# Kernel tuning notes

Measured on AMD Instinct MI355X. Metric: run time of the kernel, lower is better.

The kernel has to match this reference:

```python
import jax, jax.numpy as jnp
import numpy as np

N = 50000          # nodes
E = 800000         # edges (before self loops)
IN_C = 64
HID = 32
HEADS = 4
HC = HID * HEADS   # 128
OUT_C = 3
NEG_SLOPE = 0.2


def _lin(key, fan_out, fan_in, scale=None):
    if scale is None:
        scale = 1.0 / np.sqrt(fan_in)
    return (jax.random.normal(key, (fan_out, fan_in), dtype=jnp.float32) * scale)


def setup_inputs() -> dict:
    key = jax.random.key(0)
    ks = jax.random.split(key, 24)
    inp = {
        "x": jax.random.normal(ks[0], (N, IN_C), dtype=jnp.float32),
        "edge_index": jax.random.randint(ks[1], (2, E), 0, N, dtype=jnp.int64),
        "edge_attr": jax.random.uniform(ks[2], (E,), dtype=jnp.float32),
        "g1_Wl": _lin(ks[3], HC, IN_C), "g1_bl": jnp.zeros((HC,), jnp.float32),
        "g1_Wr": _lin(ks[4], HC, IN_C), "g1_br": jnp.zeros((HC,), jnp.float32),
        "g1_We": _lin(ks[5], HC, 1),
        "g1_att": jax.random.normal(ks[6], (HEADS, HID), dtype=jnp.float32) / np.sqrt(HID),
        "g1_bias": jnp.zeros((HC,), jnp.float32),
        "g2_Wl": _lin(ks[7], HC, HC), "g2_bl": jnp.zeros((HC,), jnp.float32),
        "g2_Wr": _lin(ks[8], HC, HC), "g2_br": jnp.zeros((HC,), jnp.float32),
        "g2_We": _lin(ks[9], HC, 1),
        "g2_att": jax.random.normal(ks[10], (1, HC), dtype=jnp.float32) / np.sqrt(HC),
        "g2_bias": jnp.zeros((HC,), jnp.float32),
        # residual projection (in_channels != hidden*heads)
        "res1_W": _lin(ks[11], HC, IN_C), "res1_b": jnp.zeros((HC,), jnp.float32),
        # MLP head
        "fc1_W": _lin(ks[12], HID, HC), "fc1_b": jnp.zeros((HID,), jnp.float32),
        "fc2_W": _lin(ks[13], 32, HID), "fc2_b": jnp.zeros((32,), jnp.float32),
        "fc3_W": _lin(ks[14], OUT_C, 32), "fc3_b": jnp.zeros((OUT_C,), jnp.float32),
    }
    return inp


def gatv2_conv(x, src, dst, ea, Wl, bl, Wr, br, We, att, bias, heads, out_c):
    # x: [N, F]; src/dst: [E'] (self loops already appended); ea: [E', 1]
    xl = (x @ Wl.T + bl).reshape(N, heads, out_c)   # lin_l -> source features
    xr = (x @ Wr.T + br).reshape(N, heads, out_c)   # lin_r -> target features
    ee = (ea @ We.T).reshape(-1, heads, out_c)      # lin_edge (no bias)
    xj = xl[src]                                    # [E', H, C] gather
    m = jax.nn.leaky_relu(xj + xr[dst] + ee, NEG_SLOPE)
    alpha = jnp.einsum('ehc,hc->eh', m, att)        # per-edge logits
    amax = jax.ops.segment_max(alpha, dst, num_segments=N)
    ex = jnp.exp(alpha - amax[dst])
    denom = jax.ops.segment_sum(ex, dst, num_segments=N)
    alpha = ex / (denom[dst] + 1e-16)               # segment softmax over incoming edges
    out = jax.ops.segment_sum(xj * alpha[..., None], dst, num_segments=N)
    return out.reshape(N, heads * out_c) + bias


def reference(x, edge_index, edge_attr,
              g1_Wl, g1_bl, g1_Wr, g1_br, g1_We, g1_att, g1_bias,
              g2_Wl, g2_bl, g2_Wr, g2_br, g2_We, g2_att, g2_bias,
              res1_W, res1_b, fc1_W, fc1_b, fc2_W, fc2_b, fc3_W, fc3_b):
    ea = edge_attr.reshape(-1, 1)                   # dim()==1 -> view(-1,1)
    # add self loops; edge_attr fill_value='mean' (PyG default)
    loop = jnp.arange(N)
    src = jnp.concatenate([edge_index[0], loop])
    dst = jnp.concatenate([edge_index[1], loop])
    ea_mean = jnp.mean(ea, axis=0, keepdims=True)
    ea_full = jnp.concatenate([ea, jnp.broadcast_to(ea_mean, (N, 1))], axis=0)

    h = gatv2_conv(x, src, dst, ea_full, g1_Wl, g1_bl, g1_Wr, g1_br,
                   g1_We, g1_att, g1_bias, HEADS, HID)
    h = jax.nn.elu(h + (x @ res1_W.T + res1_b))     # residual (projected) + ELU

    h2 = gatv2_conv(h, src, dst, ea_full, g2_Wl, g2_bl, g2_Wr, g2_br,
                    g2_We, g2_att, g2_bias, 1, HC)
    h2 = jax.nn.elu(h2 + h)                         # identity residual + ELU

    y = jax.nn.relu(h2 @ fc1_W.T + fc1_b)
    y = jax.nn.relu(y @ fc2_W.T + fc2_b)
    return y @ fc3_W.T + fc3_b                      # [N, 3]
```

## Files before the change

kernel.cpp:

```cpp
#include <hip/hip_runtime.h>
#include <math.h>


typedef short s16x8 __attribute__((ext_vector_type(8)));
typedef float f32x4 __attribute__((ext_vector_type(4)));
typedef float f32x2 __attribute__((ext_vector_type(2)));

__device__ inline unsigned short f2bf(float x) {
  unsigned int u = __float_as_uint(x);
  return (unsigned short)((u + 0x7fffu + ((u >> 16) & 1u)) >> 16);
}
__device__ inline float bf2f(unsigned short h) {
  return __uint_as_float(((unsigned int)h) << 16);
}
__device__ inline float bflo(unsigned int u) { return __uint_as_float(u << 16); }
__device__ inline float bfhi(unsigned int u) { return __uint_as_float(u & 0xffff0000u); }

template <int CTRL>
__device__ inline float dpp_addf(float x) {
  int y = __builtin_amdgcn_update_dpp(0, __float_as_int(x), CTRL, 0xf, 0xf, false);
  return x + __int_as_float(y);
}

__global__ __launch_bounds__(256) void hist_mean(
    const int* __restrict__ ei, const float* __restrict__ ea,
    int* __restrict__ hist, float* __restrict__ partials,
    int E, int Ep, int CH, int NB) {
  __shared__ int h[256];
  __shared__ float red[256];
  int t = threadIdx.x, c = blockIdx.x;
  h[t] = 0;
  float s = 0.f;
  __syncthreads();
  int s0 = c * CH, e_ = min(Ep, s0 + CH);
  for (int e = s0 + t; e < e_; e += 256) {
    int d;
    if (e < E) { d = ei[E + e]; s += ea[e]; }
    else       { d = e - E; }
    atomicAdd(&h[d >> 8], 1);
  }
  red[t] = s;
  __syncthreads();
  for (int ofs = 128; ofs > 0; ofs >>= 1) {
    if (t < ofs) red[t] += red[t + ofs];
    __syncthreads();
  }
  if (t == 0) partials[c] = red[0];
  for (int k = t; k < NB; k += 256) hist[(size_t)k * gridDim.x + c] = h[k];
}

__global__ __launch_bounds__(256) void mean_final_kernel(
    const float* __restrict__ partials, float* __restrict__ meanv, int E) {
  __shared__ float red[256];
  red[threadIdx.x] = partials[threadIdx.x];
  __syncthreads();
  for (int ofs = 128; ofs > 0; ofs >>= 1) {
    if (threadIdx.x < ofs) red[threadIdx.x] += red[threadIdx.x + ofs];
    __syncthreads();
  }
  if (threadIdx.x == 0) meanv[0] = red[0] / (float)E;
}

__global__ __launch_bounds__(1024) void scan_blocksum(
    const int* __restrict__ in, int* __restrict__ blksum, int n) {
  __shared__ int ws[16];
  int t = threadIdx.x;
  int base = blockIdx.x * 4096 + t * 4;
  int s = 0;
  if (base + 3 < n) {
    int4 v = *(const int4*)(in + base);
    s = v.x + v.y + v.z + v.w;
  } else {
    for (int i = 0; i < 4; i++) if (base + i < n) s += in[base + i];
  }
  int lane = t & 63, w = t >> 6;
#pragma unroll
  for (int ofs = 1; ofs < 64; ofs <<= 1) s += __shfl_xor(s, ofs);
  if (lane == 0) ws[w] = s;
  __syncthreads();
  if (t == 0) {
    int tot = 0;
#pragma unroll
    for (int i = 0; i < 16; i++) tot += ws[i];
    blksum[blockIdx.x] = tot;
  }
}

__global__ __launch_bounds__(64) void scan_blkoff(int* __restrict__ blksum, int nb) {
  int t = threadIdx.x;
  int v = (t < nb) ? blksum[t] : 0;
  int orig = v;
#pragma unroll
  for (int ofs = 1; ofs < 64; ofs <<= 1) {
    int u = __shfl_up(v, ofs);
    if (t >= ofs) v += u;
  }
  if (t < nb) blksum[t] = v - orig;
}

__global__ __launch_bounds__(1024) void scan_out(
    const int* __restrict__ in, const int* __restrict__ blksum,
    int* __restrict__ out, int n, int total) {
  __shared__ int ws[16];
  int t = threadIdx.x;
  int base = blockIdx.x * 4096 + t * 4;
  int4 v = {0, 0, 0, 0};
  if (base + 3 < n) {
    v = *(const int4*)(in + base);
  } else {
    if (base + 0 < n) v.x = in[base + 0];
    if (base + 1 < n) v.y = in[base + 1];
    if (base + 2 < n) v.z = in[base + 2];
    if (base + 3 < n) v.w = in[base + 3];
  }
  int s = v.x + v.y + v.z + v.w;
  int lane = t & 63, w = t >> 6;
  int inc = s;
#pragma unroll
  for (int ofs = 1; ofs < 64; ofs <<= 1) {
    int u = __shfl_up(inc, ofs);
    if (lane >= ofs) inc += u;
  }
  if (lane == 63) ws[w] = inc;
  __syncthreads();
  int waveoff = 0;
#pragma unroll
  for (int i = 0; i < 16; i++) waveoff += (i < w) ? ws[i] : 0;
  int excl = blksum[blockIdx.x] + waveoff + inc - s;
  int p0 = excl, p1 = p0 + v.x, p2 = p1 + v.y, p3 = p2 + v.z;
  if (base + 0 < n) out[base + 0] = p0;
  if (base + 1 < n) out[base + 1] = p1;
  if (base + 2 < n) out[base + 2] = p2;
  if (base + 3 < n) out[base + 3] = p3;
  if (blockIdx.x == 0 && t == 0) out[n] = total;
}

__global__ __launch_bounds__(256) void bin_scatter(
    const int* __restrict__ ei, const float* __restrict__ ea,
    const float* __restrict__ meanv, const int* __restrict__ histoff,
    unsigned int* __restrict__ binmeta, unsigned char* __restrict__ bindlo,
    int E, int Ep, int CH, int NB) {
  __shared__ int off[256];
  int t = threadIdx.x, c = blockIdx.x;
  for (int k = t; k < NB; k += 256) off[k] = histoff[(size_t)k * gridDim.x + c];
  __syncthreads();
  int s = c * CH, e_ = min(Ep, s + CH);
  for (int e = s + t; e < e_; e += 256) {
    int d, src; float eav;
    if (e < E) { src = ei[e]; d = ei[E + e]; eav = ea[e]; }
    else       { src = d = e - E; eav = meanv[0]; }
    int pos = atomicAdd(&off[d >> 8], 1);
    binmeta[pos] = (unsigned int)src | ((unsigned int)f2bf(eav) << 16);
    bindlo[pos] = (unsigned char)(d & 255);
  }
}

__global__ __launch_bounds__(256) void bin_finalize(
    const unsigned int* __restrict__ binmeta, const unsigned char* __restrict__ bindlo,
    const int* __restrict__ histoff, unsigned int* __restrict__ meta,
    int* __restrict__ row_ptr, int N, int Ep, int NCHUNK, int NB) {
  __shared__ int cntl[256];
  __shared__ int ws4[4];
  int t = threadIdx.x, k = blockIdx.x;
  int kstart = histoff[(size_t)k * NCHUNK];
  int kend = (k == NB - 1) ? Ep : histoff[(size_t)(k + 1) * NCHUNK];
  cntl[t] = 0;
  __syncthreads();
  for (int i = kstart + t; i < kend; i += 256) atomicAdd(&cntl[bindlo[i]], 1);
  __syncthreads();
  int v = cntl[t];
  int lane = t & 63, w = t >> 6;
  int inc = v;
#pragma unroll
  for (int ofs = 1; ofs < 64; ofs <<= 1) {
    int u = __shfl_up(inc, ofs);
    if (lane >= ofs) inc += u;
  }
  if (lane == 63) ws4[w] = inc;
  __syncthreads();
  int waveoff = 0;
#pragma unroll
  for (int i = 0; i < 4; i++) waveoff += (i < w) ? ws4[i] : 0;
  int base = kstart + waveoff + inc - v;
  int gd = k * 256 + t;
  if (gd < N) row_ptr[gd] = base;
  if (k == 0 && t == 0) row_ptr[N] = Ep;
  __syncthreads();
  cntl[t] = base;
  __syncthreads();
  for (int i = kstart + t; i < kend; i += 256) {
    int d = bindlo[i];
    int pos = atomicAdd(&cntl[d], 1);
    meta[pos] = binmeta[i];
  }
}

template <int K, int NMAT, int INBF>
__global__ __launch_bounds__(256) void gemm_mfma(
    const void* __restrict__ Xv,
    const float* __restrict__ W0, const float* __restrict__ b0, unsigned short* __restrict__ o0,
    const float* __restrict__ W1, const float* __restrict__ b1, unsigned short* __restrict__ o1,
    const float* __restrict__ W2, const float* __restrict__ b2, unsigned short* __restrict__ o2,
    int N) {
  constexpr int KS = K / 32;
  __shared__ unsigned short Xhi[32 * K];
  __shared__ unsigned short Xlo[INBF ? 1 : 32 * K];
  int t = threadIdx.x;
  int m0 = blockIdx.x * 32;
  int which = (NMAT == 1) ? 0 : blockIdx.y;
  const float* W = (which == 0) ? W0 : (which == 1) ? W1 : W2;
  const float* bias = (which == 0) ? b0 : (which == 1) ? b1 : b2;
  unsigned short* out = (which == 0) ? o0 : (which == 1) ? o1 : o2;

  if (INBF) {
    const unsigned short* X = (const unsigned short*)Xv;
#pragma unroll
    for (int i = 0; i < K / 64; ++i) {
      int idx8 = t + i * 256;
      int row = idx8 / (K / 8);
      int k8 = idx8 % (K / 8);
      int gm = m0 + row;
      uint4 v = (gm < N) ? *(const uint4*)(X + (size_t)gm * K + k8 * 8)
                         : uint4{0u, 0u, 0u, 0u};
      int us = (row * K + k8 * 8) ^ ((row & 7) << 3);
      *(uint4*)&Xhi[us] = v;
    }
  } else {
    const float* X = (const float*)Xv;
#pragma unroll
    for (int i = 0; i < K / 32; ++i) {
      int idx4 = t + i * 256;
      int row = idx4 / (K / 4);
      int k4 = idx4 % (K / 4);
      int gm = m0 + row;
      float4 v = (gm < N) ? *(const float4*)(X + (size_t)gm * K + k4 * 4)
                          : float4{0.f, 0.f, 0.f, 0.f};
      float f[4] = {v.x, v.y, v.z, v.w};
      ushort4 h, l;
      unsigned short* hp = (unsigned short*)&h;
      unsigned short* lp = (unsigned short*)&l;
#pragma unroll
      for (int j = 0; j < 4; ++j) {
        unsigned short hb = f2bf(f[j]);
        hp[j] = hb;
        lp[j] = f2bf(f[j] - bf2f(hb));
      }
      int us = (row * K + k4 * 4) ^ ((row & 7) << 3);
      *(ushort4*)&Xhi[us] = h;
      *(ushort4*)&Xlo[us] = l;
    }
  }

  int wv = t >> 6, lane = t & 63;
  int lr = lane & 15, kg = lane >> 4;

  s16x8 Whi[2][KS], Wlo[2][KS];
#pragma unroll
  for (int ni = 0; ni < 2; ++ni) {
#pragma unroll
    for (int ks = 0; ks < KS; ++ks) {
      const float* wp = W + (size_t)(wv * 32 + ni * 16 + lr) * K + ks * 32 + kg * 8;
      float f[8];
      *(float4*)f = *(const float4*)wp;
      *(float4*)(f + 4) = *(const float4*)(wp + 4);
#pragma unroll
      for (int j = 0; j < 8; ++j) {
        unsigned short hb = f2bf(f[j]);
        Whi[ni][ks][j] = (short)hb;
        Wlo[ni][ks][j] = (short)f2bf(f[j] - bf2f(hb));
      }
    }
  }

  __syncthreads();

  f32x4 acc[2][2] = {{{0.f, 0.f, 0.f, 0.f}, {0.f, 0.f, 0.f, 0.f}},
                     {{0.f, 0.f, 0.f, 0.f}, {0.f, 0.f, 0.f, 0.f}}};
#pragma unroll
  for (int ks = 0; ks < KS; ++ks) {
#pragma unroll
    for (int mi = 0; mi < 2; ++mi) {
      int r = mi * 16 + lr;
      int us = (r * K + ks * 32 + kg * 8) ^ ((r & 7) << 3);
      s16x8 ah = *(const s16x8*)&Xhi[us];
#pragma unroll
      for (int ni = 0; ni < 2; ++ni) {
        acc[mi][ni] = __builtin_amdgcn_mfma_f32_16x16x32_bf16(ah, Whi[ni][ks], acc[mi][ni], 0, 0, 0);
        acc[mi][ni] = __builtin_amdgcn_mfma_f32_16x16x32_bf16(ah, Wlo[ni][ks], acc[mi][ni], 0, 0, 0);
      }
      if (!INBF) {
        s16x8 al = *(const s16x8*)&Xlo[us];
#pragma unroll
        for (int ni = 0; ni < 2; ++ni) {
          acc[mi][ni] = __builtin_amdgcn_mfma_f32_16x16x32_bf16(al, Whi[ni][ks], acc[mi][ni], 0, 0, 0);
        }
      }
    }
  }

#pragma unroll
  for (int ni = 0; ni < 2; ++ni) {
    int col = wv * 32 + ni * 16 + lr;
    float bv = bias[col];
#pragma unroll
    for (int mi = 0; mi < 2; ++mi) {
#pragma unroll
      for (int j = 0; j < 4; ++j) {
        int gm = m0 + mi * 16 + kg * 4 + j;
        if (gm < N) out[(size_t)gm * 128 + col] = f2bf(acc[mi][ni][j] + bv);
      }
    }
  }
}

template <int RED>
__global__ __launch_bounds__(256) void attn_kernel(
    const unsigned short* __restrict__ xl, const unsigned short* __restrict__ xr,
    const unsigned short* __restrict__ resid, const float* __restrict__ We,
    const float* __restrict__ att, const float* __restrict__ bias,
    const unsigned int* __restrict__ meta, const int* __restrict__ row_ptr,
    unsigned short* __restrict__ outbuf, int N) {
  int wid = threadIdx.x >> 6;
  int lane = threadIdx.x & 63;
  int n = blockIdx.x * 4 + wid;
  if (n >= N) return;
  int g = lane >> 4, li = lane & 15;
  int c = li * 8;
  f32x2 xr2[4], we2[4], at2[4];
  {
    uint4 xrr = *(const uint4*)(xr + (size_t)n * 128 + c);
    xr2[0] = f32x2{bflo(xrr.x), bfhi(xrr.x)};
    xr2[1] = f32x2{bflo(xrr.y), bfhi(xrr.y)};
    xr2[2] = f32x2{bflo(xrr.z), bfhi(xrr.z)};
    xr2[3] = f32x2{bflo(xrr.w), bfhi(xrr.w)};
  }
#pragma unroll
  for (int j = 0; j < 4; j++) {
    we2[j] = *(const f32x2*)(We + c + 2 * j);
    at2[j] = *(const f32x2*)(att + c + 2 * j) * 1.44269504088896f;
  }
  int rs = row_ptr[n], re = row_ptr[n + 1];
  float s = 0.f;
  f32x2 acc2[4] = {{0.f, 0.f}, {0.f, 0.f}, {0.f, 0.f}, {0.f, 0.f}};
  int nit = (re - rs + 3) >> 2;
  int idx = rs + g;
  bool v0 = idx < re;
  unsigned int md0 = meta[v0 ? idx : rs];
  int i1 = idx + 4;
  bool v1 = i1 < re;
  unsigned int md1 = meta[v1 ? i1 : rs];
  int i2 = idx + 8;
  bool v2 = i2 < re;
  unsigned int md2 = meta[v2 ? i2 : rs];
  uint4 raw0 = *(const uint4*)(xl + (size_t)(md0 & 0xFFFFu) * 128 + c);
  uint4 raw1 = *(const uint4*)(xl + (size_t)(md1 & 0xFFFFu) * 128 + c);
  for (int it = 0; it < nit; ++it) {
    int i3 = idx + 12;
    bool v3 = i3 < re;
    unsigned int md3 = meta[v3 ? i3 : rs];
    uint4 raw2 = *(const uint4*)(xl + (size_t)(md2 & 0xFFFFu) * 128 + c);
    f32x2 xa2[4];
    xa2[0] = f32x2{bflo(raw0.x), bfhi(raw0.x)};
    xa2[1] = f32x2{bflo(raw0.y), bfhi(raw0.y)};
    xa2[2] = f32x2{bflo(raw0.z), bfhi(raw0.z)};
    xa2[3] = f32x2{bflo(raw0.w), bfhi(raw0.w)};
    float eavf = __uint_as_float(md0 & 0xffff0000u);
    f32x2 eav2 = {eavf, eavf};
    f32x2 p2 = {0.f, 0.f};
#pragma unroll
    for (int j = 0; j < 4; j++) {
      f32x2 t = xa2[j] + xr2[j];
      t = eav2 * we2[j] + t;
      f32x2 u = t * 0.2f;
      t = __builtin_elementwise_max(t, u);
      p2 = t * at2[j] + p2;
    }
    float p = p2.x + p2.y;
    p = dpp_addf<0xB1>(p);
    p = dpp_addf<0x4E>(p);
    if (RED == 16) {
      p = dpp_addf<0x141>(p);
      p = dpp_addf<0x140>(p);
    }
    float ex = v0 ? exp2f(p) : 0.f;
    f32x2 ex2 = {ex, ex};
    s += ex;
#pragma unroll
    for (int j = 0; j < 4; j++) acc2[j] = ex2 * xa2[j] + acc2[j];
    idx += 4;
    v0 = v1; v1 = v2; v2 = v3;
    md0 = md1; md1 = md2; md2 = md3;
    raw0 = raw1; raw1 = raw2;
  }
#pragma unroll
  for (int ofs = 16; ofs <= 32; ofs <<= 1) {
    s += __shfl_xor(s, ofs);
#pragma unroll
    for (int j = 0; j < 4; j++) {
      acc2[j].x += __shfl_xor(acc2[j].x, ofs);
      acc2[j].y += __shfl_xor(acc2[j].y, ofs);
    }
  }
  if (g == 0) {
    float inv = 1.f / (s + 1e-16f);
    uint4 rr = *(const uint4*)(resid + (size_t)n * 128 + c);
    float rv[8];
    rv[0] = bflo(rr.x); rv[1] = bfhi(rr.x);
    rv[2] = bflo(rr.y); rv[3] = bfhi(rr.y);
    rv[4] = bflo(rr.z); rv[5] = bfhi(rr.z);
    rv[6] = bflo(rr.w); rv[7] = bfhi(rr.w);
    float o[8];
#pragma unroll
    for (int j = 0; j < 4; j++) {
      f32x2 bi = *(const f32x2*)(bias + c + 2 * j);
      o[2 * j]     = acc2[j].x * inv + bi.x + rv[2 * j];
      o[2 * j + 1] = acc2[j].y * inv + bi.y + rv[2 * j + 1];
    }
#pragma unroll
    for (int j = 0; j < 8; j++) o[j] = (o[j] > 0.f) ? o[j] : (__expf(o[j]) - 1.f);
    uint4 pk;
    pk.x = (unsigned int)f2bf(o[0]) | ((unsigned int)f2bf(o[1]) << 16);
    pk.y = (unsigned int)f2bf(o[2]) | ((unsigned int)f2bf(o[3]) << 16);
    pk.z = (unsigned int)f2bf(o[4]) | ((unsigned int)f2bf(o[5]) << 16);
    pk.w = (unsigned int)f2bf(o[6]) | ((unsigned int)f2bf(o[7]) << 16);
    *(uint4*)(outbuf + (size_t)n * 128 + c) = pk;
  }
}

__global__ __launch_bounds__(256) void mlp_kernel(
    const unsigned short* __restrict__ h2,
    const float* __restrict__ W1, const float* __restrict__ b1,
    const float* __restrict__ W2, const float* __restrict__ b2,
    const float* __restrict__ W3, const float* __restrict__ b3,
    float* __restrict__ out, int N) {
  __shared__ float w1t[128][33];
  __shared__ float w2t[32][33];
  __shared__ float w3t[32][4];
  __shared__ float hs[8][132];
  __shared__ float y1s[8][33];
  __shared__ float y2s[8][33];
  int t = threadIdx.x;
  int n0 = blockIdx.x * 8;
  for (int idx = t; idx < 4096; idx += 256) {
    int oc = idx >> 7, k = idx & 127;
    w1t[k][oc] = W1[idx];
  }
  for (int idx = t; idx < 1024; idx += 256) {
    int oc = idx >> 5, k = idx & 31;
    w2t[k][oc] = W2[idx];
  }
  if (t < 96) {
    int oc = t >> 5, k = t & 31;
    w3t[k][oc] = W3[t];
  }
  if (t < 128) {
    int nl = t >> 4, k8 = t & 15;
    int gm = n0 + nl;
    uint4 v = (gm < N) ? *(const uint4*)(h2 + (size_t)gm * 128 + k8 * 8)
                       : uint4{0u, 0u, 0u, 0u};
    float* hp = &hs[nl][k8 * 8];
    hp[0] = bflo(v.x); hp[1] = bfhi(v.x);
    hp[2] = bflo(v.y); hp[3] = bfhi(v.y);
    hp[4] = bflo(v.z); hp[5] = bfhi(v.z);
    hp[6] = bflo(v.w); hp[7] = bfhi(v.w);
  }
  __syncthreads();
  int nl = t >> 5, oc = t & 31;
  int n = n0 + nl;
  float acc = b1[oc];
#pragma unroll 8
  for (int k = 0; k < 128; k++) acc += hs[nl][k] * w1t[k][oc];
  y1s[nl][oc] = fmaxf(acc, 0.f);
  float acc2 = b2[oc];
#pragma unroll
  for (int k = 0; k < 32; k++) acc2 += y1s[nl][k] * w2t[k][oc];
  y2s[nl][oc] = fmaxf(acc2, 0.f);
  if (oc < 3 && n < N) {
    float acc3 = b3[oc];
#pragma unroll
    for (int k = 0; k < 32; k++) acc3 += y2s[nl][k] * w3t[k][oc];
    out[(size_t)n * 3 + oc] = acc3;
  }
}

extern "C" void kernel_launch(void* const* d_in, const int* in_sizes, int n_in,
                              void* d_out, int out_size, void* d_ws, size_t ws_size,
                              hipStream_t stream) {
  const float* x      = (const float*)d_in[0];
  const int*   ei     = (const int*)d_in[1];
  const float* ea     = (const float*)d_in[2];
  const float* g1_Wl  = (const float*)d_in[3];
  const float* g1_bl  = (const float*)d_in[4];
  const float* g1_Wr  = (const float*)d_in[5];
  const float* g1_br  = (const float*)d_in[6];
  const float* g1_We  = (const float*)d_in[7];
  const float* g1_att = (const float*)d_in[8];
  const float* g1_bias= (const float*)d_in[9];
  const float* g2_Wl  = (const float*)d_in[10];
  const float* g2_bl  = (const float*)d_in[11];
  const float* g2_Wr  = (const float*)d_in[12];
  const float* g2_br  = (const float*)d_in[13];
  const float* g2_We  = (const float*)d_in[14];
  const float* g2_att = (const float*)d_in[15];
  const float* g2_bias= (const float*)d_in[16];
  const float* res1_W = (const float*)d_in[17];
  const float* res1_b = (const float*)d_in[18];
  const float* fc1_W  = (const float*)d_in[19];
  const float* fc1_b  = (const float*)d_in[20];
  const float* fc2_W  = (const float*)d_in[21];
  const float* fc2_b  = (const float*)d_in[22];
  const float* fc3_W  = (const float*)d_in[23];
  const float* fc3_b  = (const float*)d_in[24];
  float* out = (float*)d_out;

  int N = in_sizes[0] / 64;
  int E = in_sizes[2];
  int Ep = E + N;

  const int NCHUNK = 256;
  int CH = (Ep + NCHUNK - 1) / NCHUNK;
  int NB = (N + 255) >> 8;
  int Nh = NB * NCHUNK;

  char* ws = (char*)d_ws;
  size_t off = 0;
  auto carve = [&](size_t bytes) -> char* {
    char* p = ws + off;
    off = (off + bytes + 255) & ~(size_t)255;
    return p;
  };
  float* meanv    = (float*)carve(4);
  float* partials = (float*)carve(NCHUNK * 4);
  int*   blksum   = (int*)carve(64 * 4);
  int*   hist     = (int*)carve((size_t)(Nh + 1) * 4);
  int*   histoff  = (int*)carve((size_t)(Nh + 1) * 4);
  int*   row_ptr  = (int*)carve((size_t)(N + 1) * 4);
  unsigned int* binmeta = (unsigned int*)carve((size_t)Ep * 4);
  unsigned char* bindlo = (unsigned char*)carve((size_t)Ep);
  unsigned int* meta = (unsigned int*)carve((size_t)Ep * 4);
  unsigned short* xlbf = (unsigned short*)carve((size_t)N * 128 * 2);
  unsigned short* xrbf = (unsigned short*)carve((size_t)N * 128 * 2);
  unsigned short* resh2 = (unsigned short*)carve((size_t)N * 128 * 2);
  unsigned short* hbuf = (unsigned short*)carve((size_t)N * 128 * 2);
  (void)ws_size; (void)n_in; (void)out_size;

  hist_mean<<<NCHUNK, 256, 0, stream>>>(ei, ea, hist, partials, E, Ep, CH, NB);
  mean_final_kernel<<<1, 256, 0, stream>>>(partials, meanv, E);
  int nbscan = (Nh + 4095) / 4096;
  scan_blocksum<<<nbscan, 1024, 0, stream>>>(hist, blksum, Nh);
  scan_blkoff<<<1, 64, 0, stream>>>(blksum, nbscan);
  scan_out<<<nbscan, 1024, 0, stream>>>(hist, blksum, histoff, Nh, Ep);
  bin_scatter<<<NCHUNK, 256, 0, stream>>>(ei, ea, meanv, histoff, binmeta,
                                          bindlo, E, Ep, CH, NB);
  bin_finalize<<<NB, 256, 0, stream>>>(binmeta, bindlo, histoff, meta,
                                       row_ptr, N, Ep, NCHUNK, NB);

  int mblk32 = (N + 31) / 32;
  gemm_mfma<64, 3, 0><<<dim3(mblk32, 3), 256, 0, stream>>>(
      x, g1_Wl, g1_bl, xlbf, g1_Wr, g1_br, xrbf, res1_W, res1_b, resh2, N);
  attn_kernel<4><<<(N + 3) / 4, 256, 0, stream>>>(
      xlbf, xrbf, resh2, g1_We, g1_att, g1_bias, meta, row_ptr, hbuf, N);
  gemm_mfma<128, 2, 1><<<dim3(mblk32, 2), 256, 0, stream>>>(
      hbuf, g2_Wl, g2_bl, xlbf, g2_Wr, g2_br, xrbf, (const float*)nullptr,
      (const float*)nullptr, (unsigned short*)nullptr, N);
  attn_kernel<16><<<(N + 3) / 4, 256, 0, stream>>>(
      xlbf, xrbf, hbuf, g2_We, g2_att, g2_bias, meta, row_ptr, resh2, N);
  mlp_kernel<<<(N + 7) / 8, 256, 0, stream>>>(resh2, fc1_W, fc1_b, fc2_W, fc2_b,
                                              fc3_W, fc3_b, out, N);
}
```

Measured before the change: 251.4 us.

## Precompute bf16 weight splits, merge small kernels, enlarge GEMM and MLP tiles

Adds a wprep kernel that splits all GEMM weights into bf16 hi/lo once per call, so each GEMM block loads precomputed bf16 fragments instead of converting fp32 weights. The mean-reduction kernel is merged into the block-offset scan kernel, which removes one launch. GEMM blocks now cover 64 rows instead of 32, and the MLP kernel handles 32 nodes per 1024-thread block instead of 8 nodes per 256-thread block. These changes amortise the per-block weight load and conversion and reduce launch count, at the cost of one extra kernel launch, more LDS per block and fewer blocks.

```diff
diff --git a/kernel.cpp b/kernel.cpp
--- a/kernel.cpp
+++ b/kernel.cpp
@@ -20,6 +20,24 @@
 __device__ inline float dpp_addf(float x) {
   int y = __builtin_amdgcn_update_dpp(0, __float_as_int(x), CTRL, 0xf, 0xf, false);
   return x + __int_as_float(y);
+}
+
+__global__ __launch_bounds__(256) void wprep(
+    const float* __restrict__ g1wl, const float* __restrict__ g1wr,
+    const float* __restrict__ res1w, const float* __restrict__ g2wl,
+    const float* __restrict__ g2wr,
+    unsigned short* __restrict__ hi, unsigned short* __restrict__ lo) {
+  int i = blockIdx.x * 256 + threadIdx.x;
+  if (i >= 57344) return;
+  float f;
+  if (i < 8192) f = g1wl[i];
+  else if (i < 16384) f = g1wr[i - 8192];
+  else if (i < 24576) f = res1w[i - 16384];
+  else if (i < 40960) f = g2wl[i - 24576];
+  else f = g2wr[i - 40960];
+  unsigned short h = f2bf(f);
+  hi[i] = h;
+  lo[i] = f2bf(f - bf2f(h));
 }
 
 __global__ __launch_bounds__(256) void hist_mean(
@@ -47,18 +65,6 @@
   }
   if (t == 0) partials[c] = red[0];
   for (int k = t; k < NB; k += 256) hist[(size_t)k * gridDim.x + c] = h[k];
-}
-
-__global__ __launch_bounds__(256) void mean_final_kernel(
-    const float* __restrict__ partials, float* __restrict__ meanv, int E) {
-  __shared__ float red[256];
-  red[threadIdx.x] = partials[threadIdx.x];
-  __syncthreads();
-  for (int ofs = 128; ofs > 0; ofs >>= 1) {
-    if (threadIdx.x < ofs) red[threadIdx.x] += red[threadIdx.x + ofs];
-    __syncthreads();
-  }
-  if (threadIdx.x == 0) meanv[0] = red[0] / (float)E;
 }
 
 __global__ __launch_bounds__(1024) void scan_blocksum(
@@ -86,16 +92,26 @@
   }
 }
 
-__global__ __launch_bounds__(64) void scan_blkoff(int* __restrict__ blksum, int nb) {
+__global__ __launch_bounds__(128) void blkoff_mean(
+    int* __restrict__ blksum, int nb,
+    const float* __restrict__ partials, float* __restrict__ meanv, int E) {
   int t = threadIdx.x;
-  int v = (t < nb) ? blksum[t] : 0;
-  int orig = v;
-#pragma unroll
-  for (int ofs = 1; ofs < 64; ofs <<= 1) {
-    int u = __shfl_up(v, ofs);
-    if (t >= ofs) v += u;
-  }
-  if (t < nb) blksum[t] = v - orig;
+  if (t < 64) {
+    int v = (t < nb) ? blksum[t] : 0;
+    int orig = v;
+#pragma unroll
+    for (int ofs = 1; ofs < 64; ofs <<= 1) {
+      int u = __shfl_up(v, ofs);
+      if (t >= ofs) v += u;
+    }
+    if (t < nb) blksum[t] = v - orig;
+  } else {
+    int l = t - 64;
+    float s = partials[l] + partials[l + 64] + partials[l + 128] + partials[l + 192];
+#pragma unroll
+    for (int ofs = 1; ofs < 64; ofs <<= 1) s += __shfl_xor(s, ofs);
+    if (l == 0) meanv[0] = s / (float)E;
+  }
 }
 
 __global__ __launch_bounds__(1024) void scan_out(
@@ -198,24 +214,25 @@
 template <int K, int NMAT, int INBF>
 __global__ __launch_bounds__(256) void gemm_mfma(
     const void* __restrict__ Xv,
-    const float* __restrict__ W0, const float* __restrict__ b0, unsigned short* __restrict__ o0,
-    const float* __restrict__ W1, const float* __restrict__ b1, unsigned short* __restrict__ o1,
-    const float* __restrict__ W2, const float* __restrict__ b2, unsigned short* __restrict__ o2,
+    const unsigned short* __restrict__ Whi_all, const unsigned short* __restrict__ Wlo_all,
+    int off0, const float* __restrict__ b0, unsigned short* __restrict__ o0,
+    int off1, const float* __restrict__ b1, unsigned short* __restrict__ o1,
+    int off2, const float* __restrict__ b2, unsigned short* __restrict__ o2,
     int N) {
   constexpr int KS = K / 32;
-  __shared__ unsigned short Xhi[32 * K];
-  __shared__ unsigned short Xlo[INBF ? 1 : 32 * K];
+  __shared__ unsigned short Xhi[64 * K];
+  __shared__ unsigned short Xlo[INBF ? 1 : 64 * K];
   int t = threadIdx.x;
-  int m0 = blockIdx.x * 32;
+  int m0 = blockIdx.x * 64;
   int which = (NMAT == 1) ? 0 : blockIdx.y;
-  const float* W = (which == 0) ? W0 : (which == 1) ? W1 : W2;
+  int woff = (which == 0) ? off0 : (which == 1) ? off1 : off2;
   const float* bias = (which == 0) ? b0 : (which == 1) ? b1 : b2;
   unsigned short* out = (which == 0) ? o0 : (which == 1) ? o1 : o2;
 
   if (INBF) {
     const unsigned short* X = (const unsigned short*)Xv;
 #pragma unroll
-    for (int i = 0; i < K / 64; ++i) {
+    for (int i = 0; i < K / 32; ++i) {
       int idx8 = t + i * 256;
       int row = idx8 / (K / 8);
       int k8 = idx8 % (K / 8);
@@ -228,7 +245,7 @@
   } else {
     const float* X = (const float*)Xv;
 #pragma unroll
-    for (int i = 0; i < K / 32; ++i) {
+    for (int i = 0; i < K / 16; ++i) {
       int idx4 = t + i * 256;
       int row = idx4 / (K / 4);
       int k4 = idx4 % (K / 4);
@@ -254,45 +271,39 @@
   int wv = t >> 6, lane = t & 63;
   int lr = lane & 15, kg = lane >> 4;
 
-  s16x8 Whi[2][KS], Wlo[2][KS];
+  s16x8 Whf[2][KS], Wlf[2][KS];
+  const unsigned short* Wh = Whi_all + woff;
+  const unsigned short* Wl = Wlo_all + woff;
 #pragma unroll
   for (int ni = 0; ni < 2; ++ni) {
 #pragma unroll
     for (int ks = 0; ks < KS; ++ks) {
-      const float* wp = W + (size_t)(wv * 32 + ni * 16 + lr) * K + ks * 32 + kg * 8;
-      float f[8];
-      *(float4*)f = *(const float4*)wp;
-      *(float4*)(f + 4) = *(const float4*)(wp + 4);
-#pragma unroll
-      for (int j = 0; j < 8; ++j) {
-        unsigned short hb = f2bf(f[j]);
-        Whi[ni][ks][j] = (short)hb;
-        Wlo[ni][ks][j] = (short)f2bf(f[j] - bf2f(hb));
-      }
-    }
-  }
-
-  __syncthreads();
-
-  f32x4 acc[2][2] = {{{0.f, 0.f, 0.f, 0.f}, {0.f, 0.f, 0.f, 0.f}},
-                     {{0.f, 0.f, 0.f, 0.f}, {0.f, 0.f, 0.f, 0.f}}};
+      int widx = (wv * 32 + ni * 16 + lr) * K + ks * 32 + kg * 8;
+      Whf[ni][ks] = *(const s16x8*)(Wh + widx);
+      Wlf[ni][ks] = *(const s16x8*)(Wl + widx);
+    }
+  }
+
+  __syncthreads();
+
+  f32x4 acc[4][2] = {};
 #pragma unroll
   for (int ks = 0; ks < KS; ++ks) {
 #pragma unroll
-    for (int mi = 0; mi < 2; ++mi) {
+    for (int mi = 0; mi < 4; ++mi) {
       int r = mi * 16 + lr;
       int us = (r * K + ks * 32 + kg * 8) ^ ((r & 7) << 3);
       s16x8 ah = *(const s16x8*)&Xhi[us];
 #pragma unroll
       for (int ni = 0; ni < 2; ++ni) {
-        acc[mi][ni] = __builtin_amdgcn_mfma_f32_16x16x32_bf16(ah, Whi[ni][ks], acc[mi][ni], 0, 0, 0);
-        acc[mi][ni] = __builtin_amdgcn_mfma_f32_16x16x32_bf16(ah, Wlo[ni][ks], acc[mi][ni], 0, 0, 0);
+        acc[mi][ni] = __builtin_amdgcn_mfma_f32_16x16x32_bf16(ah, Whf[ni][ks], acc[mi][ni], 0, 0, 0);
+        acc[mi][ni] = __builtin_amdgcn_mfma_f32_16x16x32_bf16(ah, Wlf[ni][ks], acc[mi][ni], 0, 0, 0);
       }
       if (!INBF) {
         s16x8 al = *(const s16x8*)&Xlo[us];
 #pragma unroll
         for (int ni = 0; ni < 2; ++ni) {
-          acc[mi][ni] = __builtin_amdgcn_mfma_f32_16x16x32_bf16(al, Whi[ni][ks], acc[mi][ni], 0, 0, 0);
+          acc[mi][ni] = __builtin_amdgcn_mfma_f32_16x16x32_bf16(al, Whf[ni][ks], acc[mi][ni], 0, 0, 0);
         }
       }
     }
@@ -303,7 +314,7 @@
     int col = wv * 32 + ni * 16 + lr;
     float bv = bias[col];
 #pragma unroll
-    for (int mi = 0; mi < 2; ++mi) {
+    for (int mi = 0; mi < 4; ++mi) {
 #pragma unroll
       for (int j = 0; j < 4; ++j) {
         int gm = m0 + mi * 16 + kg * 4 + j;
@@ -427,7 +438,7 @@
   }
 }
 
-__global__ __launch_bounds__(256) void mlp_kernel(
+__global__ __launch_bounds__(1024) void mlp_kernel(
     const unsigned short* __restrict__ h2,
     const float* __restrict__ W1, const float* __restrict__ b1,
     const float* __restrict__ W2, const float* __restrict__ b2,
@@ -436,24 +447,24 @@
   __shared__ float w1t[128][33];
   __shared__ float w2t[32][33];
   __shared__ float w3t[32][4];
-  __shared__ float hs[8][132];
-  __shared__ float y1s[8][33];
-  __shared__ float y2s[8][33];
+  __shared__ float hs[32][132];
+  __shared__ float y1s[32][33];
+  __shared__ float y2s[32][33];
   int t = threadIdx.x;
-  int n0 = blockIdx.x * 8;
-  for (int idx = t; idx < 4096; idx += 256) {
+  int n0 = blockIdx.x * 32;
+  for (int idx = t; idx < 4096; idx += 1024) {
     int oc = idx >> 7, k = idx & 127;
     w1t[k][oc] = W1[idx];
   }
-  for (int idx = t; idx < 1024; idx += 256) {
-    int oc = idx >> 5, k = idx & 31;
-    w2t[k][oc] = W2[idx];
+  {
+    int oc = t >> 5, k = t & 31;
+    w2t[k][oc] = W2[t];
   }
   if (t < 96) {
     int oc = t >> 5, k = t & 31;
     w3t[k][oc] = W3[t];
   }
-  if (t < 128) {
+  if (t < 512) {
     int nl = t >> 4, k8 = t & 15;
     int gm = n0 + nl;
     uint4 v = (gm < N) ? *(const uint4*)(h2 + (size_t)gm * 128 + k8 * 8)
@@ -542,29 +553,31 @@
   unsigned short* xrbf = (unsigned short*)carve((size_t)N * 128 * 2);
   unsigned short* resh2 = (unsigned short*)carve((size_t)N * 128 * 2);
   unsigned short* hbuf = (unsigned short*)carve((size_t)N * 128 * 2);
+  unsigned short* Whi = (unsigned short*)carve(57344 * 2);
+  unsigned short* Wlo = (unsigned short*)carve(57344 * 2);
   (void)ws_size; (void)n_in; (void)out_size;
 
+  wprep<<<224, 256, 0, stream>>>(g1_Wl, g1_Wr, res1_W, g2_Wl, g2_Wr, Whi, Wlo);
   hist_mean<<<NCHUNK, 256, 0, stream>>>(ei, ea, hist, partials, E, Ep, CH, NB);
-  mean_final_kernel<<<1, 256, 0, stream>>>(partials, meanv, E);
   int nbscan = (Nh + 4095) / 4096;
   scan_blocksum<<<nbscan, 1024, 0, stream>>>(hist, blksum, Nh);
-  scan_blkoff<<<1, 64, 0, stream>>>(blksum, nbscan);
+  blkoff_mean<<<1, 128, 0, stream>>>(blksum, nbscan, partials, meanv, E);
   scan_out<<<nbscan, 1024, 0, stream>>>(hist, blksum, histoff, Nh, Ep);
   bin_scatter<<<NCHUNK, 256, 0, stream>>>(ei, ea, meanv, histoff, binmeta,
                                           bindlo, E, Ep, CH, NB);
   bin_finalize<<<NB, 256, 0, stream>>>(binmeta, bindlo, histoff, meta,
                                        row_ptr, N, Ep, NCHUNK, NB);
 
-  int mblk32 = (N + 31) / 32;
-  gemm_mfma<64, 3, 0><<<dim3(mblk32, 3), 256, 0, stream>>>(
-      x, g1_Wl, g1_bl, xlbf, g1_Wr, g1_br, xrbf, res1_W, res1_b, resh2, N);
+  int mblk64 = (N + 63) / 64;
+  gemm_mfma<64, 3, 0><<<dim3(mblk64, 3), 256, 0, stream>>>(
+      x, Whi, Wlo, 0, g1_bl, xlbf, 8192, g1_br, xrbf, 16384, res1_b, resh2, N);
   attn_kernel<4><<<(N + 3) / 4, 256, 0, stream>>>(
       xlbf, xrbf, resh2, g1_We, g1_att, g1_bias, meta, row_ptr, hbuf, N);
-  gemm_mfma<128, 2, 1><<<dim3(mblk32, 2), 256, 0, stream>>>(
-      hbuf, g2_Wl, g2_bl, xlbf, g2_Wr, g2_br, xrbf, (const float*)nullptr,
+  gemm_mfma<128, 2, 1><<<dim3(mblk64, 2), 256, 0, stream>>>(
+      hbuf, Whi, Wlo, 24576, g2_bl, xlbf, 40960, g2_br, xrbf, 0,
       (const float*)nullptr, (unsigned short*)nullptr, N);
   attn_kernel<16><<<(N + 3) / 4, 256, 0, stream>>>(
       xlbf, xrbf, hbuf, g2_We, g2_att, g2_bias, meta, row_ptr, resh2, N);
-  mlp_kernel<<<(N + 7) / 8, 256, 0, stream>>>(resh2, fc1_W, fc1_b, fc2_W, fc2_b,
-                                              fc3_W, fc3_b, out, N);
-}
+  mlp_kernel<<<(N + 31) / 32, 1024, 0, stream>>>(resh2, fc1_W, fc1_b, fc2_W,
+                                                 fc2_b, fc3_W, fc3_b, out, N);
+}
```

After: 243.5 us. 1.03x faster.
